# Kernel optimization log

Measured on AMD Instinct MI355X. Metric: run time of the kernel, lower is better.

Reference implementation:

```python
import jax, jax.numpy as jnp
import numpy as np

B, S, D = 4, 2048, 1024  # batch, seq_len, d_model


def setup_inputs() -> dict:
    key = jax.random.key(0)
    k0, k1, k2, k3 = jax.random.split(key, 4)
    x = jax.random.normal(k0, (B, S, D), dtype=jnp.float32)
    W_Q = jax.random.normal(k1, (D, D), dtype=jnp.float32) * (D ** -0.5)
    W_K = jax.random.normal(k2, (D, D), dtype=jnp.float32) * (D ** -0.5)
    W_V = jax.random.normal(k3, (D, D), dtype=jnp.float32) * (D ** -0.5)
    return {"x": x, "W_Q": W_Q, "W_K": W_K, "W_V": W_V}


def reference(x, W_Q, W_K, W_V):
    # Q/K/V projections: input @ W.t()
    Q = jnp.matmul(x, W_Q.T)  # [B,S,D]
    K = jnp.matmul(x, W_K.T)  # [B,S,D]
    V = jnp.matmul(x, W_V.T)  # [B,S,D]
    b, s, d = K.shape
    # Faithful to original: a row-major RESHAPE of K (not a transpose!)
    K_r = K.reshape(b, d, s)  # [B,D,S]
    scores = jnp.matmul(Q, K_r) / d  # divided by d_model (not sqrt), per source
    attn = jax.nn.softmax(scores, axis=-1)  # [B,S,S]
    return jnp.matmul(attn, V)  # [B,S,D]
```

## Files before the change

### kernel.cpp

```cpp
#include <hip/hip_runtime.h>
#include <hip/hip_bf16.h>
#include <stdint.h>

#define BB 4
#define SS 2048
#define DD 1024

typedef __attribute__((ext_vector_type(4))) float f32x4;
typedef __attribute__((ext_vector_type(8))) __bf16 bf16x8;

typedef const __attribute__((address_space(1))) void* gptr_t;
typedef __attribute__((address_space(3))) void* lptr_t;

__device__ __forceinline__ void load_lds16(const void* g, void* l) {
  __builtin_amdgcn_global_load_lds((gptr_t)g, (lptr_t)l, 16, 0, 0);
}

__device__ __forceinline__ unsigned short f2bf(float x) {
  union { float f; uint32_t u; } v; v.f = x;
  uint32_t u = v.u;
  return (unsigned short)((u + 0x7FFFu + ((u >> 16) & 1u)) >> 16);
}
__device__ __forceinline__ float bf2f(unsigned short h) {
  union { uint32_t u; float f; } v; v.u = ((uint32_t)h) << 16; return v.f;
}

__global__ __launch_bounds__(256) void convert_x(
    const float* __restrict__ in, unsigned short* __restrict__ out, int n4) {
  for (int i = blockIdx.x * 256 + threadIdx.x; i < n4; i += gridDim.x * 256) {
    float4 v = ((const float4*)in)[i];
    ushort4 o;
    o.x = f2bf(v.x); o.y = f2bf(v.y); o.z = f2bf(v.z); o.w = f2bf(v.w);
    ((ushort4*)out)[i] = o;
  }
}

__global__ __launch_bounds__(256) void convert_w(
    const float* __restrict__ wq, const float* __restrict__ wk,
    const float* __restrict__ wv, unsigned short* __restrict__ wcat) {
  const int n4 = DD * DD / 4;
  int i = blockIdx.x * 256 + threadIdx.x;
  const int which = i / n4, j = i - which * n4;
  const float* src = (which == 0) ? wq : ((which == 1) ? wk : wv);
  float4 v = ((const float4*)src)[j];
  ushort4 o;
  o.x = f2bf(v.x); o.y = f2bf(v.y); o.z = f2bf(v.z); o.w = f2bf(v.w);
  ((ushort4*)(wcat + (size_t)which * DD * DD))[j] = o;
}

__device__ __forceinline__ void gemm_core_128(
    const unsigned short* __restrict__ A, const unsigned short* __restrict__ Bt,
    int K, int lda, int ldb, int row0, int col0,
    unsigned short* As, unsigned short* Bs, f32x4 acc[4][4]) {
  const int tid  = threadIdx.x;
  const int lane = tid & 63;
  const int wave = tid >> 6;
  const int wm = wave >> 1, wn = wave & 1;

#pragma unroll
  for (int i = 0; i < 4; ++i)
#pragma unroll
    for (int j = 0; j < 4; ++j) acc[i][j] = (f32x4)(0.f);

  const unsigned short* aS0 = A  + (size_t)(row0 + wave * 16 + (lane >> 2)) * lda + (lane & 3) * 8;
  const unsigned short* aS1 = aS0 + (size_t)64 * lda;
  const unsigned short* bS0 = Bt + (size_t)(col0 + wave * 16 + (lane >> 2)) * ldb + (lane & 3) * 8;
  const unsigned short* bS1 = bS0 + (size_t)64 * ldb;
  unsigned short* lA0 = As + wave * 512;
  unsigned short* lA1 = As + (wave + 4) * 512;
  unsigned short* lB0 = Bs + wave * 512;
  unsigned short* lB1 = Bs + (wave + 4) * 512;

  const unsigned short* arow = As + ((wm * 64 + (lane & 15)) * 32) + (lane >> 4) * 8;
  const unsigned short* brow = Bs + ((wn * 64 + (lane & 15)) * 32) + (lane >> 4) * 8;

  for (int k0 = 0; k0 < K; k0 += 32) {
    load_lds16(aS0 + k0, lA0);
    load_lds16(aS1 + k0, lA1);
    load_lds16(bS0 + k0, lB0);
    load_lds16(bS1 + k0, lB1);
    __syncthreads();

    bf16x8 af[4], bf[4];
#pragma unroll
    for (int fm = 0; fm < 4; ++fm) af[fm] = *(const bf16x8*)(arow + fm * 512);
#pragma unroll
    for (int fn = 0; fn < 4; ++fn) bf[fn] = *(const bf16x8*)(brow + fn * 512);
#pragma unroll
    for (int fm = 0; fm < 4; ++fm)
#pragma unroll
      for (int fn = 0; fn < 4; ++fn)
        acc[fm][fn] = __builtin_amdgcn_mfma_f32_16x16x32_bf16(af[fm], bf[fn], acc[fm][fn], 0, 0, 0);
    __syncthreads();
  }
}

__global__ __launch_bounds__(256) void proj_gemm(
    const unsigned short* __restrict__ xb, const unsigned short* __restrict__ wcat,
    unsigned short* __restrict__ q, unsigned short* __restrict__ kk, unsigned short* __restrict__ vv) {
  __shared__ __align__(16) unsigned short As[128 * 32];
  __shared__ __align__(16) unsigned short Bs[128 * 32];
  f32x4 acc[4][4];
  const int bm = blockIdx.y, bn = blockIdx.x;
  gemm_core_128(xb, wcat, 1024, 1024, 1024, bm * 128, bn * 128, As, Bs, acc);

  const int tid = threadIdx.x, lane = tid & 63, wave = tid >> 6;
  const int wm = wave >> 1, wn = wave & 1;
  const int which = bn >> 3;
  unsigned short* dst = (which == 0) ? q : ((which == 1) ? kk : vv);
  const int cb = (bn & 7) * 128 + wn * 64 + (lane & 15);
  const int rb = bm * 128 + wm * 64 + (lane >> 4) * 4;
#pragma unroll
  for (int fm = 0; fm < 4; ++fm)
#pragma unroll
    for (int i = 0; i < 4; ++i) {
      const size_t rowoff = (size_t)(rb + fm * 16 + i) * 1024;
#pragma unroll
      for (int fn = 0; fn < 4; ++fn)
        dst[rowoff + cb + fn * 16] = f2bf(acc[fm][fn][i]);
    }
}

__global__ __launch_bounds__(256) void k_to_mt(
    const unsigned short* __restrict__ k, unsigned short* __restrict__ mt) {
  const int z = blockIdx.z, b = z >> 1, delta = z & 1;
  const unsigned short* kb = k + (size_t)b * SS * DD + (size_t)delta * DD;
  unsigned short* mtb = mt + (size_t)b * SS * DD + (size_t)delta * DD * DD;
  __shared__ unsigned short tile[32][33];
  const int tx = threadIdx.x, ty = threadIdx.y;
  const int i0 = blockIdx.x * 32, j0 = blockIdx.y * 32;
#pragma unroll
  for (int yy = ty; yy < 32; yy += 8)
    tile[yy][tx] = kb[(size_t)(i0 + yy) * 2048 + j0 + tx];
  __syncthreads();
#pragma unroll
  for (int yy = ty; yy < 32; yy += 8)
    mtb[(size_t)(j0 + yy) * 1024 + i0 + tx] = tile[tx][yy];
}

__global__ __launch_bounds__(256) void v_to_vt(
    const unsigned short* __restrict__ v, unsigned short* __restrict__ vt) {
  const int b = blockIdx.z;
  const unsigned short* vb = v + (size_t)b * SS * DD;
  unsigned short* vtb = vt + (size_t)b * DD * SS;
  __shared__ unsigned short tile[32][33];
  const int tx = threadIdx.x, ty = threadIdx.y;
  const int k0 = blockIdx.x * 32, n0 = blockIdx.y * 32;
#pragma unroll
  for (int yy = ty; yy < 32; yy += 8)
    tile[yy][tx] = vb[(size_t)(k0 + yy) * 1024 + n0 + tx];
  __syncthreads();
#pragma unroll
  for (int yy = ty; yy < 32; yy += 8)
    vtb[(size_t)(n0 + yy) * 2048 + k0 + tx] = tile[tx][yy];
}

__global__ __launch_bounds__(256) void score_gemm(
    const unsigned short* __restrict__ q, const unsigned short* __restrict__ mt,
    unsigned short* __restrict__ sc) {
  __shared__ __align__(16) unsigned short As[128 * 32];
  __shared__ __align__(16) unsigned short Bs[128 * 32];
  f32x4 acc[4][4];
  const int b = blockIdx.z;
  gemm_core_128(q + (size_t)b * SS * DD, mt + (size_t)b * SS * DD,
                1024, 1024, 1024, blockIdx.y * 128, blockIdx.x * 128, As, Bs, acc);
  unsigned short* out = sc + (size_t)b * SS * SS;
  const int tid = threadIdx.x, lane = tid & 63, wave = tid >> 6;
  const int wm = wave >> 1, wn = wave & 1;
  const int cb = blockIdx.x * 128 + wn * 64 + (lane & 15);
  const int rb = blockIdx.y * 128 + wm * 64 + (lane >> 4) * 4;
  const float scale = 1.0f / 1024.0f;
#pragma unroll
  for (int fm = 0; fm < 4; ++fm)
#pragma unroll
    for (int i = 0; i < 4; ++i) {
      const size_t rowoff = (size_t)(rb + fm * 16 + i) * 2048;
#pragma unroll
      for (int fn = 0; fn < 4; ++fn)
        out[rowoff + cb + fn * 16] = f2bf(acc[fm][fn][i] * scale);
    }
}

__global__ __launch_bounds__(256) void softmax_kernel(unsigned short* __restrict__ sc) {
  const size_t row = blockIdx.x;
  unsigned short* io = sc + row * 2048;
  const int t = threadIdx.x;
  ushort4 u0 = ((const ushort4*)io)[t];
  ushort4 u1 = ((const ushort4*)io)[t + 256];
  float v[8];
  v[0] = bf2f(u0.x); v[1] = bf2f(u0.y); v[2] = bf2f(u0.z); v[3] = bf2f(u0.w);
  v[4] = bf2f(u1.x); v[5] = bf2f(u1.y); v[6] = bf2f(u1.z); v[7] = bf2f(u1.w);
  float m = v[0];
#pragma unroll
  for (int j = 1; j < 8; ++j) m = fmaxf(m, v[j]);
#pragma unroll
  for (int off = 32; off > 0; off >>= 1) m = fmaxf(m, __shfl_xor(m, off));
  __shared__ float redm[4], reds[4];
  const int w = t >> 6;
  if ((t & 63) == 0) redm[w] = m;
  __syncthreads();
  m = fmaxf(fmaxf(redm[0], redm[1]), fmaxf(redm[2], redm[3]));
  float s = 0.f;
#pragma unroll
  for (int j = 0; j < 8; ++j) { v[j] = __expf(v[j] - m); s += v[j]; }
#pragma unroll
  for (int off = 32; off > 0; off >>= 1) s += __shfl_xor(s, off);
  if ((t & 63) == 0) reds[w] = s;
  __syncthreads();
  const float inv = 1.0f / (reds[0] + reds[1] + reds[2] + reds[3]);
  ushort4 o0, o1;
  o0.x = f2bf(v[0] * inv); o0.y = f2bf(v[1] * inv); o0.z = f2bf(v[2] * inv); o0.w = f2bf(v[3] * inv);
  o1.x = f2bf(v[4] * inv); o1.y = f2bf(v[5] * inv); o1.z = f2bf(v[6] * inv); o1.w = f2bf(v[7] * inv);
  ((ushort4*)io)[t] = o0;
  ((ushort4*)io)[t + 256] = o1;
}

__global__ __launch_bounds__(256) void pv_gemm(
    const unsigned short* __restrict__ p, const unsigned short* __restrict__ vt,
    float* __restrict__ out) {
  __shared__ __align__(16) unsigned short As[128 * 32];
  __shared__ __align__(16) unsigned short Bs[128 * 32];
  f32x4 acc[4][4];
  const int b = blockIdx.z;
  gemm_core_128(p + (size_t)b * SS * SS, vt + (size_t)b * DD * SS,
                2048, 2048, 2048, blockIdx.y * 128, blockIdx.x * 128, As, Bs, acc);
  float* ob = out + (size_t)b * SS * DD;
  const int tid = threadIdx.x, lane = tid & 63, wave = tid >> 6;
  const int wm = wave >> 1, wn = wave & 1;
  const int cb = blockIdx.x * 128 + wn * 64 + (lane & 15);
  const int rb = blockIdx.y * 128 + wm * 64 + (lane >> 4) * 4;
#pragma unroll
  for (int fm = 0; fm < 4; ++fm)
#pragma unroll
    for (int i = 0; i < 4; ++i) {
      const size_t rowoff = (size_t)(rb + fm * 16 + i) * 1024;
#pragma unroll
      for (int fn = 0; fn < 4; ++fn)
        ob[rowoff + cb + fn * 16] = acc[fm][fn][i];
    }
}

extern "C" void kernel_launch(void* const* d_in, const int* in_sizes, int n_in,
                              void* d_out, int out_size, void* d_ws, size_t ws_size,
                              hipStream_t stream) {
  const float* x  = (const float*)d_in[0];
  const float* wq = (const float*)d_in[1];
  const float* wk = (const float*)d_in[2];
  const float* wv = (const float*)d_in[3];
  float* out = (float*)d_out;
  uint8_t* ws = (uint8_t*)d_ws;

  const size_t MB = 1u << 20;
  unsigned short* xb   = (unsigned short*)(ws);
  unsigned short* wcat = (unsigned short*)(ws + 16 * MB);
  unsigned short* q    = (unsigned short*)(ws + 22 * MB);
  unsigned short* kk   = (unsigned short*)(ws + 38 * MB);
  unsigned short* vv   = (unsigned short*)(ws + 54 * MB);
  unsigned short* mt   = (unsigned short*)(ws + 70 * MB);
  unsigned short* vt   = (unsigned short*)(ws + 86 * MB);
  unsigned short* sc   = (unsigned short*)(ws + 102 * MB);

  convert_x<<<2048, 256, 0, stream>>>(x, xb, BB * SS * DD / 4);
  convert_w<<<3 * DD * DD / 4 / 256, 256, 0, stream>>>(wq, wk, wv, wcat);
  proj_gemm<<<dim3(24, 64), 256, 0, stream>>>(xb, wcat, q, kk, vv);
  k_to_mt<<<dim3(32, 32, 8), dim3(32, 8), 0, stream>>>(kk, mt);
  v_to_vt<<<dim3(64, 32, 4), dim3(32, 8), 0, stream>>>(vv, vt);
  score_gemm<<<dim3(16, 16, 4), 256, 0, stream>>>(q, mt, sc);
  softmax_kernel<<<BB * SS, 256, 0, stream>>>(sc);
  pv_gemm<<<dim3(8, 16, 4), 256, 0, stream>>>(sc, vt, out);
}
```

Measured before the change: 295.3 us.

## Rewrite GEMM core with double-buffered LDS, swizzle, and larger tiles

Replaces the single-buffered 128x128 GEMM core with a templated 512-thread core. It double-buffers 64-wide K stages in dynamic LDS with an XOR swizzle, uses explicit vmcnt waits, sched barriers and setprio, and splits each K stage into two MFMA halves. Tiles grow to 128x256 or 256x256, aiming to overlap global loads with compute, raise data reuse and reduce bank conflicts. In exchange it uses far more LDS (96-128 KB per block) and relies on hand-placed waits being correct.

```diff
diff --git a/kernel.cpp b/kernel.cpp
--- a/kernel.cpp
+++ b/kernel.cpp
@@ -14,6 +14,18 @@
 
 __device__ __forceinline__ void load_lds16(const void* g, void* l) {
   __builtin_amdgcn_global_load_lds((gptr_t)g, (lptr_t)l, 16, 0, 0);
+}
+
+#define SBAR0() __builtin_amdgcn_sched_barrier(0)
+
+template <int N>
+__device__ __forceinline__ void wait_vmcnt() {
+  if constexpr (N == 0) asm volatile("s_waitcnt vmcnt(0)" ::: "memory");
+  else if constexpr (N == 6) asm volatile("s_waitcnt vmcnt(6)" ::: "memory");
+  else if constexpr (N == 8) asm volatile("s_waitcnt vmcnt(8)" ::: "memory");
+}
+__device__ __forceinline__ void wait_lgkm0() {
+  asm volatile("s_waitcnt lgkmcnt(0)" ::: "memory");
 }
 
 __device__ __forceinline__ unsigned short f2bf(float x) {
@@ -48,76 +60,123 @@
   ((ushort4*)(wcat + (size_t)which * DD * DD))[j] = o;
 }
 
-__device__ __forceinline__ void gemm_core_128(
+template <int BM, int KLEN>
+__device__ __forceinline__ void gemm_core(
     const unsigned short* __restrict__ A, const unsigned short* __restrict__ Bt,
-    int K, int lda, int ldb, int row0, int col0,
-    unsigned short* As, unsigned short* Bs, f32x4 acc[4][4]) {
+    int lda, int ldb, int row0, int col0, char* lds,
+    f32x4 (&acc)[BM / 32][4]) {
+  constexpr int M_REP = BM / 32;
+  constexpr int NT   = KLEN / 64;
+  constexpr int ASZ  = BM * 128;
+  constexpr int BUFSZ = ASZ + 32768;
+  constexpr int LPT  = (BM + 256) / 64;
+  constexpr int NA   = BM / 64;
+
   const int tid  = threadIdx.x;
   const int lane = tid & 63;
-  const int wave = tid >> 6;
-  const int wm = wave >> 1, wn = wave & 1;
-
-#pragma unroll
-  for (int i = 0; i < 4; ++i)
-#pragma unroll
-    for (int j = 0; j < 4; ++j) acc[i][j] = (f32x4)(0.f);
-
-  const unsigned short* aS0 = A  + (size_t)(row0 + wave * 16 + (lane >> 2)) * lda + (lane & 3) * 8;
-  const unsigned short* aS1 = aS0 + (size_t)64 * lda;
-  const unsigned short* bS0 = Bt + (size_t)(col0 + wave * 16 + (lane >> 2)) * ldb + (lane & 3) * 8;
-  const unsigned short* bS1 = bS0 + (size_t)64 * ldb;
-  unsigned short* lA0 = As + wave * 512;
-  unsigned short* lA1 = As + (wave + 4) * 512;
-  unsigned short* lB0 = Bs + wave * 512;
-  unsigned short* lB1 = Bs + (wave + 4) * 512;
-
-  const unsigned short* arow = As + ((wm * 64 + (lane & 15)) * 32) + (lane >> 4) * 8;
-  const unsigned short* brow = Bs + ((wn * 64 + (lane & 15)) * 32) + (lane >> 4) * 8;
-
-  for (int k0 = 0; k0 < K; k0 += 32) {
-    load_lds16(aS0 + k0, lA0);
-    load_lds16(aS1 + k0, lA1);
-    load_lds16(bS0 + k0, lB0);
-    load_lds16(bS1 + k0, lB1);
-    __syncthreads();
-
-    bf16x8 af[4], bf[4];
-#pragma unroll
-    for (int fm = 0; fm < 4; ++fm) af[fm] = *(const bf16x8*)(arow + fm * 512);
-#pragma unroll
-    for (int fn = 0; fn < 4; ++fn) bf[fn] = *(const bf16x8*)(brow + fn * 512);
-#pragma unroll
-    for (int fm = 0; fm < 4; ++fm)
-#pragma unroll
-      for (int fn = 0; fn < 4; ++fn)
-        acc[fm][fn] = __builtin_amdgcn_mfma_f32_16x16x32_bf16(af[fm], bf[fn], acc[fm][fn], 0, 0, 0);
-    __syncthreads();
+  const int w    = tid >> 6;
+  const int wr = w >> 2, wc = w & 3;
+
+#pragma unroll
+  for (int f = 0; f < M_REP; ++f)
+#pragma unroll
+    for (int n = 0; n < 4; ++n) acc[f][n] = (f32x4)(0.f);
+
+  const int l8 = lane >> 3, l7 = lane & 7;
+  const int swz = l7 ^ l8;
+  const unsigned short* srcA = A  + (size_t)(row0 + w * (BM / 8) + l8) * lda + swz * 8;
+  const unsigned short* srcB = Bt + (size_t)(col0 + w * 32 + l8) * ldb + swz * 8;
+  char* ldsAw = lds + w * (BM / 8) * 128;
+  char* ldsBw = lds + ASZ + w * 4096;
+
+  const int l15 = lane & 15, l16 = lane >> 4;
+  const int xc0 = ((l16) ^ l7) * 16;
+  const int xc1 = ((4 + l16) ^ l7) * 16;
+  const char* rdA = lds + wr * (BM / 2) * 128 + l15 * 128;
+  const char* rdB = lds + ASZ + wc * 8192 + l15 * 128;
+
+  auto STAGE = [&](int kt) {
+    const unsigned short* a = srcA + kt * 64;
+    const unsigned short* b = srcB + kt * 64;
+    char* la = ldsAw + (kt & 1) * BUFSZ;
+    char* lb = ldsBw + (kt & 1) * BUFSZ;
+#pragma unroll
+    for (int c = 0; c < NA; ++c) load_lds16(a + (size_t)c * 8 * lda, la + c * 1024);
+#pragma unroll
+    for (int c = 0; c < 4; ++c)  load_lds16(b + (size_t)c * 8 * ldb, lb + c * 1024);
+  };
+
+  STAGE(0);
+  STAGE(1);
+
+#pragma unroll 1
+  for (int t = 0; t < NT; ++t) {
+    if (t == NT - 1) wait_vmcnt<0>(); else wait_vmcnt<LPT>();
+    SBAR0();
+    __builtin_amdgcn_s_barrier();
+    SBAR0();
+
+    const char* pA = rdA + (t & 1) * BUFSZ;
+    const char* pB = rdB + (t & 1) * BUFSZ;
+
+    bf16x8 a0[M_REP], b0[4], a1[M_REP], b1[4];
+#pragma unroll
+    for (int n = 0; n < 4; ++n) b0[n] = *(const bf16x8*)(pB + xc0 + n * 2048);
+#pragma unroll
+    for (int f = 0; f < M_REP; ++f) a0[f] = *(const bf16x8*)(pA + xc0 + f * 2048);
+
+    __builtin_amdgcn_s_setprio(1);
+#pragma unroll
+    for (int f = 0; f < M_REP; ++f)
+#pragma unroll
+      for (int n = 0; n < 4; ++n)
+        acc[f][n] = __builtin_amdgcn_mfma_f32_16x16x32_bf16(a0[f], b0[n], acc[f][n], 0, 0, 0);
+    __builtin_amdgcn_s_setprio(0);
+
+#pragma unroll
+    for (int n = 0; n < 4; ++n) b1[n] = *(const bf16x8*)(pB + xc1 + n * 2048);
+#pragma unroll
+    for (int f = 0; f < M_REP; ++f) a1[f] = *(const bf16x8*)(pA + xc1 + f * 2048);
+
+    wait_lgkm0();
+    SBAR0();
+    __builtin_amdgcn_s_barrier();
+    SBAR0();
+    if (t + 2 < NT) STAGE(t + 2);
+
+    __builtin_amdgcn_s_setprio(1);
+#pragma unroll
+    for (int f = 0; f < M_REP; ++f)
+#pragma unroll
+      for (int n = 0; n < 4; ++n)
+        acc[f][n] = __builtin_amdgcn_mfma_f32_16x16x32_bf16(a1[f], b1[n], acc[f][n], 0, 0, 0);
+    __builtin_amdgcn_s_setprio(0);
   }
 }
 
-__global__ __launch_bounds__(256) void proj_gemm(
+__global__ __launch_bounds__(512, 2) void proj_gemm(
     const unsigned short* __restrict__ xb, const unsigned short* __restrict__ wcat,
-    unsigned short* __restrict__ q, unsigned short* __restrict__ kk, unsigned short* __restrict__ vv) {
-  __shared__ __align__(16) unsigned short As[128 * 32];
-  __shared__ __align__(16) unsigned short Bs[128 * 32];
+    unsigned short* __restrict__ q, unsigned short* __restrict__ kk,
+    unsigned short* __restrict__ vv) {
+  extern __shared__ char lds[];
   f32x4 acc[4][4];
-  const int bm = blockIdx.y, bn = blockIdx.x;
-  gemm_core_128(xb, wcat, 1024, 1024, 1024, bm * 128, bn * 128, As, Bs, acc);
-
-  const int tid = threadIdx.x, lane = tid & 63, wave = tid >> 6;
-  const int wm = wave >> 1, wn = wave & 1;
-  const int which = bn >> 3;
+  const int bn = blockIdx.x, bm = blockIdx.y;
+  gemm_core<128, 1024>(xb, wcat, 1024, 1024, bm * 128, bn * 256, lds, acc);
+
+  const int lane = threadIdx.x & 63, w = threadIdx.x >> 6;
+  const int wr = w >> 2, wc = w & 3;
+  const int which = bn >> 2;
   unsigned short* dst = (which == 0) ? q : ((which == 1) ? kk : vv);
-  const int cb = (bn & 7) * 128 + wn * 64 + (lane & 15);
-  const int rb = bm * 128 + wm * 64 + (lane >> 4) * 4;
-#pragma unroll
-  for (int fm = 0; fm < 4; ++fm)
+  const int colb = (bn & 3) * 256 + wc * 64 + (lane & 15);
+  const int rowb = bm * 128 + wr * 64 + (lane >> 4) * 4;
+#pragma unroll
+  for (int f = 0; f < 4; ++f)
 #pragma unroll
     for (int i = 0; i < 4; ++i) {
-      const size_t rowoff = (size_t)(rb + fm * 16 + i) * 1024;
-#pragma unroll
-      for (int fn = 0; fn < 4; ++fn)
-        dst[rowoff + cb + fn * 16] = f2bf(acc[fm][fn][i]);
+      const size_t rowoff = (size_t)(rowb + f * 16 + i) * 1024;
+#pragma unroll
+      for (int n = 0; n < 4; ++n)
+        dst[rowoff + colb + n * 16] = f2bf(acc[f][n][i]);
     }
 }
 
@@ -155,29 +214,28 @@
     vtb[(size_t)(n0 + yy) * 2048 + k0 + tx] = tile[tx][yy];
 }
 
-__global__ __launch_bounds__(256) void score_gemm(
+__global__ __launch_bounds__(512, 2) void score_gemm(
     const unsigned short* __restrict__ q, const unsigned short* __restrict__ mt,
     unsigned short* __restrict__ sc) {
-  __shared__ __align__(16) unsigned short As[128 * 32];
-  __shared__ __align__(16) unsigned short Bs[128 * 32];
-  f32x4 acc[4][4];
+  extern __shared__ char lds[];
+  f32x4 acc[8][4];
   const int b = blockIdx.z;
-  gemm_core_128(q + (size_t)b * SS * DD, mt + (size_t)b * SS * DD,
-                1024, 1024, 1024, blockIdx.y * 128, blockIdx.x * 128, As, Bs, acc);
+  gemm_core<256, 1024>(q + (size_t)b * SS * DD, mt + (size_t)b * SS * DD,
+                       1024, 1024, blockIdx.y * 256, blockIdx.x * 256, lds, acc);
   unsigned short* out = sc + (size_t)b * SS * SS;
-  const int tid = threadIdx.x, lane = tid & 63, wave = tid >> 6;
-  const int wm = wave >> 1, wn = wave & 1;
-  const int cb = blockIdx.x * 128 + wn * 64 + (lane & 15);
-  const int rb = blockIdx.y * 128 + wm * 64 + (lane >> 4) * 4;
+  const int lane = threadIdx.x & 63, w = threadIdx.x >> 6;
+  const int wr = w >> 2, wc = w & 3;
+  const int colb = blockIdx.x * 256 + wc * 64 + (lane & 15);
+  const int rowb = blockIdx.y * 256 + wr * 128 + (lane >> 4) * 4;
   const float scale = 1.0f / 1024.0f;
 #pragma unroll
-  for (int fm = 0; fm < 4; ++fm)
+  for (int f = 0; f < 8; ++f)
 #pragma unroll
     for (int i = 0; i < 4; ++i) {
-      const size_t rowoff = (size_t)(rb + fm * 16 + i) * 2048;
-#pragma unroll
-      for (int fn = 0; fn < 4; ++fn)
-        out[rowoff + cb + fn * 16] = f2bf(acc[fm][fn][i] * scale);
+      const size_t rowoff = (size_t)(rowb + f * 16 + i) * 2048;
+#pragma unroll
+      for (int n = 0; n < 4; ++n)
+        out[rowoff + colb + n * 16] = f2bf(acc[f][n][i] * scale);
     }
 }
 
@@ -215,28 +273,27 @@
   ((ushort4*)io)[t + 256] = o1;
 }
 
-__global__ __launch_bounds__(256) void pv_gemm(
+__global__ __launch_bounds__(512, 2) void pv_gemm(
     const unsigned short* __restrict__ p, const unsigned short* __restrict__ vt,
     float* __restrict__ out) {
-  __shared__ __align__(16) unsigned short As[128 * 32];
-  __shared__ __align__(16) unsigned short Bs[128 * 32];
+  extern __shared__ char lds[];
   f32x4 acc[4][4];
   const int b = blockIdx.z;
-  gemm_core_128(p + (size_t)b * SS * SS, vt + (size_t)b * DD * SS,
-                2048, 2048, 2048, blockIdx.y * 128, blockIdx.x * 128, As, Bs, acc);
+  gemm_core<128, 2048>(p + (size_t)b * SS * SS, vt + (size_t)b * DD * SS,
+                       2048, 2048, blockIdx.y * 128, blockIdx.x * 256, lds, acc);
   float* ob = out + (size_t)b * SS * DD;
-  const int tid = threadIdx.x, lane = tid & 63, wave = tid >> 6;
-  const int wm = wave >> 1, wn = wave & 1;
-  const int cb = blockIdx.x * 128 + wn * 64 + (lane & 15);
-  const int rb = blockIdx.y * 128 + wm * 64 + (lane >> 4) * 4;
-#pragma unroll
-  for (int fm = 0; fm < 4; ++fm)
+  const int lane = threadIdx.x & 63, w = threadIdx.x >> 6;
+  const int wr = w >> 2, wc = w & 3;
+  const int colb = blockIdx.x * 256 + wc * 64 + (lane & 15);
+  const int rowb = blockIdx.y * 128 + wr * 64 + (lane >> 4) * 4;
+#pragma unroll
+  for (int f = 0; f < 4; ++f)
 #pragma unroll
     for (int i = 0; i < 4; ++i) {
-      const size_t rowoff = (size_t)(rb + fm * 16 + i) * 1024;
-#pragma unroll
-      for (int fn = 0; fn < 4; ++fn)
-        ob[rowoff + cb + fn * 16] = acc[fm][fn][i];
+      const size_t rowoff = (size_t)(rowb + f * 16 + i) * 1024;
+#pragma unroll
+      for (int n = 0; n < 4; ++n)
+        ob[rowoff + colb + n * 16] = acc[f][n][i];
     }
 }
 
@@ -262,10 +319,10 @@
 
   convert_x<<<2048, 256, 0, stream>>>(x, xb, BB * SS * DD / 4);
   convert_w<<<3 * DD * DD / 4 / 256, 256, 0, stream>>>(wq, wk, wv, wcat);
-  proj_gemm<<<dim3(24, 64), 256, 0, stream>>>(xb, wcat, q, kk, vv);
+  proj_gemm<<<dim3(12, 64), 512, 96 * 1024, stream>>>(xb, wcat, q, kk, vv);
   k_to_mt<<<dim3(32, 32, 8), dim3(32, 8), 0, stream>>>(kk, mt);
   v_to_vt<<<dim3(64, 32, 4), dim3(32, 8), 0, stream>>>(vv, vt);
-  score_gemm<<<dim3(16, 16, 4), 256, 0, stream>>>(q, mt, sc);
+  score_gemm<<<dim3(8, 8, 4), 512, 128 * 1024, stream>>>(q, mt, sc);
   softmax_kernel<<<BB * SS, 256, 0, stream>>>(sc);
-  pv_gemm<<<dim3(8, 16, 4), 256, 0, stream>>>(sc, vt, out);
-}
+  pv_gemm<<<dim3(4, 16, 4), 512, 96 * 1024, stream>>>(sc, vt, out);
+}
```

Measured after the change: 265.2 us. 10.2% less time.
